# Optimization experiments

Measured on AMD Instinct MI355X. Metric: run time of the kernel, lower is better.

The kernel has to match this reference:

```python
import jax, jax.numpy as jnp
import numpy as np

EPS = 1e-5
COMMITMENT_WEIGHT = 1.0


def setup_inputs() -> dict:
    key = jax.random.key(0)
    k1, k2 = jax.random.split(key)
    x = jax.random.normal(k1, (4, 4096, 128), dtype=jnp.float32)
    codebook = jax.random.normal(k2, (8192, 128), dtype=jnp.float32)
    return {"x": x, "codebook": codebook}


def _layernorm(x):
    # LayerNorm over last dim, elementwise_affine=False, eps=1e-5
    mu = jnp.mean(x, axis=-1, keepdims=True)
    var = jnp.mean(jnp.square(x - mu), axis=-1, keepdims=True)
    return (x - mu) * jax.lax.rsqrt(var + EPS)


def reference(x, codebook):
    b, n, d = x.shape
    xn = _layernorm(x)                      # [b, n, d]
    flat = xn.reshape(b * n, d)             # [bn, d]
    x2 = jnp.sum(flat * flat, axis=-1, keepdims=True)          # [bn, 1]
    e2 = jnp.sum(codebook * codebook, axis=-1)                  # [K]
    dots = jnp.einsum('nd,kd->nk', flat, codebook)              # [bn, K]
    distances = x2 - 2.0 * dots + e2[None, :]                   # [bn, K]
    embed_ind = jnp.argmin(distances, axis=-1)                  # [bn]
    quantize = codebook[embed_ind].reshape(b, n, d)             # gather
    embed_ind = embed_ind.reshape(b, n)
    loss = jnp.mean(jnp.square(quantize - xn)) * COMMITMENT_WEIGHT
    # straight-through
    quantize_st = xn + jax.lax.stop_gradient(quantize - xn)
    return (quantize_st, embed_ind, loss)
```

## Files before the change

kernel.cpp:

```cpp
#include <hip/hip_runtime.h>
#include <hip/hip_fp16.h>
#include <math.h>

typedef _Float16 half8   __attribute__((ext_vector_type(8)));
typedef _Float16 half2v  __attribute__((ext_vector_type(2)));
typedef float    floatx16 __attribute__((ext_vector_type(16)));

#define ROWS   16384
#define DIM    128
#define KCODES 8192
#define NSPLIT 6
#define MTILE  128
#define LOSS_SCALE (1.0f / ((float)ROWS * (float)DIM))

__device__ __forceinline__ void async_copy16(const _Float16* src, _Float16* dst_lds) {
  __builtin_amdgcn_global_load_lds((const __attribute__((address_space(1))) void*)src,
                                   (__attribute__((address_space(3))) void*)dst_lds,
                                   16, 0, 0);
}

__global__ __launch_bounds__(256) void prep_codebook(
    const float* __restrict__ cb, _Float16* __restrict__ ehg,
    _Float16* __restrict__ elg, float* __restrict__ e2g)
{
  int tid = threadIdx.x;
  int L = tid & 63;
  int row = blockIdx.x * 4 + (tid >> 6);
  const float2* cr = (const float2*)(cb + (size_t)row * DIM);
  float2 v = cr[L];
  float s2 = v.x * v.x + v.y * v.y;
  #pragma unroll
  for (int m = 1; m < 64; m <<= 1) s2 += __shfl_xor(s2, m);
  if (L == 0) e2g[row] = -0.5f * s2;
  _Float16 h0 = (_Float16)v.x, h1 = (_Float16)v.y;
  half2v hi = {h0, h1};
  half2v lo = {(_Float16)(v.x - (float)h0), (_Float16)(v.y - (float)h1)};
  ((half2v*)(ehg + (size_t)row * DIM))[L] = hi;
  ((half2v*)(elg + (size_t)row * DIM))[L] = lo;
}

__global__ __launch_bounds__(256, 3) void argmin_kernel(
    const float* __restrict__ x, const _Float16* __restrict__ ehg,
    const _Float16* __restrict__ elg, const float* __restrict__ e2g,
    float* __restrict__ best_part, int* __restrict__ idx_part,
    float* __restrict__ x2g)
{
  __shared__ _Float16 ebuf[2][2][32][128];
  __shared__ float e2s[1376];

  int tid = threadIdx.x;
  int w   = tid >> 6;
  int L   = tid & 63;
  int col = L & 31;
  int kh  = L >> 5;

  int bx = blockIdx.x;
  int mt = bx & 127;
  int ns = bx >> 7;
  const int soff[7] = {0, 1376, 2752, 4128, 5504, 6848, 8192};
  int code0 = soff[ns];
  int ntile = (soff[ns + 1] - code0) >> 5;

  int rowbase = mt * MTILE + w * 32;
  int row = rowbase + col;

  for (int i = tid; i < soff[ns + 1] - code0; i += 256) e2s[i] = e2g[code0 + i];

  const float* xr = x + (size_t)row * DIM + kh * 8;
  float v[64];
  #pragma unroll
  for (int ks = 0; ks < 8; ++ks) {
    float4 p0 = *(const float4*)(xr + ks * 16);
    float4 p1 = *(const float4*)(xr + ks * 16 + 4);
    v[ks*8+0] = p0.x; v[ks*8+1] = p0.y; v[ks*8+2] = p0.z; v[ks*8+3] = p0.w;
    v[ks*8+4] = p1.x; v[ks*8+5] = p1.y; v[ks*8+6] = p1.z; v[ks*8+7] = p1.w;
  }
  float s = 0.f;
  #pragma unroll
  for (int i = 0; i < 64; ++i) s += v[i];
  s += __shfl_xor(s, 32);
  float mu = s * (1.0f / 128.0f);
  float s2 = 0.f;
  #pragma unroll
  for (int i = 0; i < 64; ++i) { float d = v[i] - mu; s2 += d * d; }
  s2 += __shfl_xor(s2, 32);
  float rstd = 1.0f / sqrtf(s2 * (1.0f / 128.0f) + 1e-5f);

  half8 ah[8], al[8];
  float x2 = 0.f;
  #pragma unroll
  for (int ks = 0; ks < 8; ++ks)
    #pragma unroll
    for (int j = 0; j < 8; ++j) {
      float xv = (v[ks*8+j] - mu) * rstd;
      x2 += xv * xv;
      _Float16 h = (_Float16)xv;
      ah[ks][j] = h;
      al[ks][j] = (_Float16)(xv - (float)h);
    }
  x2 += __shfl_xor(x2, 32);
  if (ns == 0 && kh == 0) x2g[row] = x2;

  float best[16]; int bch[16];
  #pragma unroll
  for (int r = 0; r < 16; ++r) { best[r] = -3.4e38f; bch[r] = 0; }

  auto stage = [&](int ch, int p) {
    int cbase = code0 + ch * 32;
    _Float16* lb = &ebuf[p][0][0][0];
    #pragma unroll
    for (int it = 0; it < 4; ++it) {
      int cid = it * 256 + tid;
      int arr = cid >> 9;
      int lc  = cid & 511;
      int n   = lc >> 4;
      int cs  = lc & 15;
      int cg  = cs ^ (n & 15);
      const _Float16* g = (arr ? elg : ehg) + (size_t)(cbase + n) * DIM + cg * 8;
      async_copy16(g, lb + (size_t)cid * 8);
    }
  };

  stage(0, 0);
  __syncthreads();

  for (int ch = 0; ch < ntile; ++ch) {
    int p = ch & 1;
    if (ch + 1 < ntile) stage(ch + 1, p ^ 1);

    float e2f = e2s[ch * 32 + col];

    floatx16 a0 = {0,0,0,0,0,0,0,0,0,0,0,0,0,0,0,0};
    floatx16 a1 = {0,0,0,0,0,0,0,0,0,0,0,0,0,0,0,0};
    #pragma unroll
    for (int ks = 0; ks < 8; ++ks) {
      int slot = (((ks << 1) | kh) ^ (col & 15)) * 8;
      half8 bh = *(const half8*)&ebuf[p][0][col][slot];
      half8 bl = *(const half8*)&ebuf[p][1][col][slot];
      a0 = __builtin_amdgcn_mfma_f32_32x32x16_f16(ah[ks], bh, a0, 0, 0, 0);
      a1 = __builtin_amdgcn_mfma_f32_32x32x16_f16(ah[ks], bl, a1, 0, 0, 0);
      a1 = __builtin_amdgcn_mfma_f32_32x32x16_f16(al[ks], bh, a1, 0, 0, 0);
    }
    #pragma unroll
    for (int r = 0; r < 16; ++r) {
      float t = (a0[r] + a1[r]) + e2f;
      if (t > best[r]) { best[r] = t; bch[r] = ch; }
    }
    __syncthreads();
  }

  int ibase = code0 + col;
  #pragma unroll
  for (int r = 0; r < 16; ++r) {
    float b = best[r];
    int   bi = (bch[r] << 5) + ibase;
    #pragma unroll
    for (int m = 1; m < 32; m <<= 1) {
      float ob = __shfl_xor(b, m);
      int   oi = __shfl_xor(bi, m);
      if (ob > b || (ob == b && oi < bi)) { b = ob; bi = oi; }
    }
    if (col == 0) {
      int rw = rowbase + (r & 3) + ((r >> 2) << 3) + (kh << 2);
      best_part[(size_t)rw * NSPLIT + ns] = b;
      idx_part [(size_t)rw * NSPLIT + ns] = bi;
    }
  }
}

__global__ __launch_bounds__(256) void gather_loss_kernel(
    const float* __restrict__ cb, const float* __restrict__ best_part,
    const int* __restrict__ idx_part, const float* __restrict__ x2g,
    float* __restrict__ out_q, float* __restrict__ out_ind,
    float* __restrict__ loss_part)
{
  __shared__ int   sidx[32];
  __shared__ float sloss[32];
  int tid = threadIdx.x;
  int rb = blockIdx.x * 32;
  int r = tid >> 3, k = tid & 7;
  int row = rb + r;

  float b  = -3.4e38f; int bi = 0x7fffffff;
  if (k < NSPLIT) {
    b  = best_part[(size_t)row * NSPLIT + k];
    bi = idx_part [(size_t)row * NSPLIT + k];
  }
  #pragma unroll
  for (int m = 1; m < 8; m <<= 1) {
    float ob = __shfl_xor(b, m);
    int   oi = __shfl_xor(bi, m);
    if (ob > b || (ob == b && oi < bi)) { b = ob; bi = oi; }
  }
  if (k == 0) {
    sidx[r] = bi;
    out_ind[row] = (float)bi;
    sloss[r] = x2g[row] - 2.0f * b;
  }
  __syncthreads();

  if (tid < 32) {
    float sl = sloss[tid];
    #pragma unroll
    for (int m = 1; m < 32; m <<= 1) sl += __shfl_xor(sl, m);
    if (tid == 0) loss_part[blockIdx.x] = sl;
  }

  const float4* cb4 = (const float4*)cb;
  float4* oq4 = (float4*)out_q;
  #pragma unroll
  for (int it = 0; it < 4; ++it) {
    int idx = it * 256 + tid;
    int r2 = idx >> 5, c4 = idx & 31;
    oq4[(size_t)(rb + r2) * 32 + c4] = cb4[(size_t)sidx[r2] * 32 + c4];
  }
}

__global__ __launch_bounds__(256) void loss_reduce_kernel(
    const float* __restrict__ loss_part, float* __restrict__ out_loss)
{
  __shared__ float sm[256];
  int tid = threadIdx.x;
  float s = loss_part[tid] + loss_part[tid + 256];
  sm[tid] = s; __syncthreads();
  for (int st = 128; st > 0; st >>= 1) {
    if (tid < st) sm[tid] += sm[tid + st];
    __syncthreads();
  }
  if (tid == 0) *out_loss = sm[0] * LOSS_SCALE;
}

extern "C" void kernel_launch(void* const* d_in, const int* in_sizes, int n_in,
                              void* d_out, int out_size, void* d_ws, size_t ws_size,
                              hipStream_t stream)
{
  const float* x  = (const float*)d_in[0];
  const float* cb = (const float*)d_in[1];

  char* ws = (char*)d_ws;
  _Float16* ehg      = (_Float16*)(ws + 0);
  _Float16* elg      = (_Float16*)(ws + 2097152);
  float*    e2g      = (float*)   (ws + 4194304);
  float*    best_part= (float*)   (ws + 4227072);
  int*      idx_part = (int*)     (ws + 4620288);
  float*    x2g      = (float*)   (ws + 5013504);
  float*    loss_part= (float*)   (ws + 5079040);

  float* out_q    = (float*)d_out;
  float* out_ind  = out_q + (size_t)ROWS * DIM;
  float* out_loss = out_ind + ROWS;

  prep_codebook<<<KCODES / 4, 256, 0, stream>>>(cb, ehg, elg, e2g);
  argmin_kernel<<<(ROWS / MTILE) * NSPLIT, 256, 0, stream>>>(x, ehg, elg, e2g, best_part, idx_part, x2g);
  gather_loss_kernel<<<ROWS / 32, 256, 0, stream>>>(cb, best_part, idx_part, x2g, out_q, out_ind, loss_part);
  loss_reduce_kernel<<<1, 256, 0, stream>>>(loss_part, out_loss);
}
```

Measured before the change: 179.3 us.

## Load codebook fragments directly from global memory, split layernorm into a prep kernel

Removes the LDS double-buffered async staging of codebook tiles. Each wave now reads its MFMA B fragments straight from global/L2 using an interleaved hi/lo fp16 layout. Layernorm and the fp16 hi/lo split of x move into a separate prep_x kernel, which writes into the output buffer as scratch. The K split drops from 6 to 4 with occupancy 2, and the gather kernel handles 64 rows per block. This removes LDS traffic and barriers, but every wave now fetches the codebook redundantly from L2, and it adds one launch.

```diff
diff --git a/kernel.cpp b/kernel.cpp
--- a/kernel.cpp
+++ b/kernel.cpp
@@ -9,25 +9,19 @@
 #define ROWS   16384
 #define DIM    128
 #define KCODES 8192
-#define NSPLIT 6
-#define MTILE  128
+#define NSPLIT 4
+#define SPLITK (KCODES / NSPLIT)
+#define NCH    (SPLITK / 32)
 #define LOSS_SCALE (1.0f / ((float)ROWS * (float)DIM))
 
-__device__ __forceinline__ void async_copy16(const _Float16* src, _Float16* dst_lds) {
-  __builtin_amdgcn_global_load_lds((const __attribute__((address_space(1))) void*)src,
-                                   (__attribute__((address_space(3))) void*)dst_lds,
-                                   16, 0, 0);
-}
-
-__global__ __launch_bounds__(256) void prep_codebook(
-    const float* __restrict__ cb, _Float16* __restrict__ ehg,
-    _Float16* __restrict__ elg, float* __restrict__ e2g)
+__global__ __launch_bounds__(256) void prep_cb(
+    const float* __restrict__ cb, _Float16* __restrict__ cbs,
+    float* __restrict__ e2g)
 {
   int tid = threadIdx.x;
   int L = tid & 63;
   int row = blockIdx.x * 4 + (tid >> 6);
-  const float2* cr = (const float2*)(cb + (size_t)row * DIM);
-  float2 v = cr[L];
+  float2 v = ((const float2*)(cb + (size_t)row * DIM))[L];
   float s2 = v.x * v.x + v.y * v.y;
   #pragma unroll
   for (int m = 1; m < 64; m <<= 1) s2 += __shfl_xor(s2, m);
@@ -35,18 +29,47 @@
   _Float16 h0 = (_Float16)v.x, h1 = (_Float16)v.y;
   half2v hi = {h0, h1};
   half2v lo = {(_Float16)(v.x - (float)h0), (_Float16)(v.y - (float)h1)};
-  ((half2v*)(ehg + (size_t)row * DIM))[L] = hi;
-  ((half2v*)(elg + (size_t)row * DIM))[L] = lo;
-}
-
-__global__ __launch_bounds__(256, 3) void argmin_kernel(
-    const float* __restrict__ x, const _Float16* __restrict__ ehg,
-    const _Float16* __restrict__ elg, const float* __restrict__ e2g,
-    float* __restrict__ best_part, int* __restrict__ idx_part,
+  _Float16* dst = cbs + (size_t)row * 256;
+  ((half2v*)dst)[L] = hi;
+  ((half2v*)(dst + 128))[L] = lo;
+}
+
+__global__ __launch_bounds__(256) void prep_x(
+    const float* __restrict__ x, _Float16* __restrict__ xs,
     float* __restrict__ x2g)
 {
-  __shared__ _Float16 ebuf[2][2][32][128];
-  __shared__ float e2s[1376];
+  int tid = threadIdx.x;
+  int L = tid & 63;
+  int row = blockIdx.x * 4 + (tid >> 6);
+  float2 v = ((const float2*)(x + (size_t)row * DIM))[L];
+  float s = v.x + v.y;
+  #pragma unroll
+  for (int m = 1; m < 64; m <<= 1) s += __shfl_xor(s, m);
+  float mu = s * (1.0f / 128.0f);
+  float dx = v.x - mu, dy = v.y - mu;
+  float s2 = dx * dx + dy * dy;
+  #pragma unroll
+  for (int m = 1; m < 64; m <<= 1) s2 += __shfl_xor(s2, m);
+  float rstd = 1.0f / sqrtf(s2 * (1.0f / 128.0f) + 1e-5f);
+  float xn0 = dx * rstd, xn1 = dy * rstd;
+  float x2 = xn0 * xn0 + xn1 * xn1;
+  #pragma unroll
+  for (int m = 1; m < 64; m <<= 1) x2 += __shfl_xor(x2, m);
+  if (L == 0) x2g[row] = x2;
+  _Float16 h0 = (_Float16)xn0, h1 = (_Float16)xn1;
+  half2v hi = {h0, h1};
+  half2v lo = {(_Float16)(xn0 - (float)h0), (_Float16)(xn1 - (float)h1)};
+  _Float16* dst = xs + (size_t)row * 256;
+  ((half2v*)dst)[L] = hi;
+  ((half2v*)(dst + 128))[L] = lo;
+}
+
+__global__ __launch_bounds__(256, 2) void argmin_kernel(
+    const _Float16* __restrict__ xs, const _Float16* __restrict__ cbs,
+    const float* __restrict__ e2g, float* __restrict__ best_part,
+    int* __restrict__ idx_part)
+{
+  __shared__ float e2s[SPLITK];
 
   int tid = threadIdx.x;
   int w   = tid >> 6;
@@ -54,99 +77,54 @@
   int col = L & 31;
   int kh  = L >> 5;
 
-  int bx = blockIdx.x;
-  int mt = bx & 127;
-  int ns = bx >> 7;
-  const int soff[7] = {0, 1376, 2752, 4128, 5504, 6848, 8192};
-  int code0 = soff[ns];
-  int ntile = (soff[ns + 1] - code0) >> 5;
-
-  int rowbase = mt * MTILE + w * 32;
-  int row = rowbase + col;
-
-  for (int i = tid; i < soff[ns + 1] - code0; i += 256) e2s[i] = e2g[code0 + i];
-
-  const float* xr = x + (size_t)row * DIM + kh * 8;
-  float v[64];
+  int mt = blockIdx.x & 127;
+  int ns = blockIdx.x >> 7;
+  int code0 = ns * SPLITK;
+
+  for (int i = tid; i < SPLITK; i += 256) e2s[i] = e2g[code0 + i];
+
+  int rowbase = mt * 128 + w * 32;
+
+  const _Float16* xa = xs + (size_t)(rowbase + col) * 256 + kh * 8;
+  half8 ah[8], al[8];
   #pragma unroll
   for (int ks = 0; ks < 8; ++ks) {
-    float4 p0 = *(const float4*)(xr + ks * 16);
-    float4 p1 = *(const float4*)(xr + ks * 16 + 4);
-    v[ks*8+0] = p0.x; v[ks*8+1] = p0.y; v[ks*8+2] = p0.z; v[ks*8+3] = p0.w;
-    v[ks*8+4] = p1.x; v[ks*8+5] = p1.y; v[ks*8+6] = p1.z; v[ks*8+7] = p1.w;
-  }
-  float s = 0.f;
-  #pragma unroll
-  for (int i = 0; i < 64; ++i) s += v[i];
-  s += __shfl_xor(s, 32);
-  float mu = s * (1.0f / 128.0f);
-  float s2 = 0.f;
-  #pragma unroll
-  for (int i = 0; i < 64; ++i) { float d = v[i] - mu; s2 += d * d; }
-  s2 += __shfl_xor(s2, 32);
-  float rstd = 1.0f / sqrtf(s2 * (1.0f / 128.0f) + 1e-5f);
-
-  half8 ah[8], al[8];
-  float x2 = 0.f;
-  #pragma unroll
-  for (int ks = 0; ks < 8; ++ks)
-    #pragma unroll
-    for (int j = 0; j < 8; ++j) {
-      float xv = (v[ks*8+j] - mu) * rstd;
-      x2 += xv * xv;
-      _Float16 h = (_Float16)xv;
-      ah[ks][j] = h;
-      al[ks][j] = (_Float16)(xv - (float)h);
-    }
-  x2 += __shfl_xor(x2, 32);
-  if (ns == 0 && kh == 0) x2g[row] = x2;
+    ah[ks] = *(const half8*)(xa + ks * 16);
+    al[ks] = *(const half8*)(xa + 128 + ks * 16);
+  }
 
   float best[16]; int bch[16];
   #pragma unroll
   for (int r = 0; r < 16; ++r) { best[r] = -3.4e38f; bch[r] = 0; }
 
-  auto stage = [&](int ch, int p) {
-    int cbase = code0 + ch * 32;
-    _Float16* lb = &ebuf[p][0][0][0];
-    #pragma unroll
-    for (int it = 0; it < 4; ++it) {
-      int cid = it * 256 + tid;
-      int arr = cid >> 9;
-      int lc  = cid & 511;
-      int n   = lc >> 4;
-      int cs  = lc & 15;
-      int cg  = cs ^ (n & 15);
-      const _Float16* g = (arr ? elg : ehg) + (size_t)(cbase + n) * DIM + cg * 8;
-      async_copy16(g, lb + (size_t)cid * 8);
-    }
-  };
-
-  stage(0, 0);
+  const _Float16* bp = cbs + (size_t)(code0 + col) * 256 + kh * 8;
+
   __syncthreads();
 
-  for (int ch = 0; ch < ntile; ++ch) {
-    int p = ch & 1;
-    if (ch + 1 < ntile) stage(ch + 1, p ^ 1);
-
+  #pragma unroll 1
+  for (int ch = 0; ch < NCH; ++ch) {
+    half8 bh[8], bl[8];
+    #pragma unroll
+    for (int ks = 0; ks < 8; ++ks) {
+      bh[ks] = *(const half8*)(bp + ks * 16);
+      bl[ks] = *(const half8*)(bp + 128 + ks * 16);
+    }
     float e2f = e2s[ch * 32 + col];
 
     floatx16 a0 = {0,0,0,0,0,0,0,0,0,0,0,0,0,0,0,0};
     floatx16 a1 = {0,0,0,0,0,0,0,0,0,0,0,0,0,0,0,0};
     #pragma unroll
     for (int ks = 0; ks < 8; ++ks) {
-      int slot = (((ks << 1) | kh) ^ (col & 15)) * 8;
-      half8 bh = *(const half8*)&ebuf[p][0][col][slot];
-      half8 bl = *(const half8*)&ebuf[p][1][col][slot];
-      a0 = __builtin_amdgcn_mfma_f32_32x32x16_f16(ah[ks], bh, a0, 0, 0, 0);
-      a1 = __builtin_amdgcn_mfma_f32_32x32x16_f16(ah[ks], bl, a1, 0, 0, 0);
-      a1 = __builtin_amdgcn_mfma_f32_32x32x16_f16(al[ks], bh, a1, 0, 0, 0);
+      a0 = __builtin_amdgcn_mfma_f32_32x32x16_f16(ah[ks], bh[ks], a0, 0, 0, 0);
+      a1 = __builtin_amdgcn_mfma_f32_32x32x16_f16(ah[ks], bl[ks], a1, 0, 0, 0);
+      a1 = __builtin_amdgcn_mfma_f32_32x32x16_f16(al[ks], bh[ks], a1, 0, 0, 0);
     }
     #pragma unroll
     for (int r = 0; r < 16; ++r) {
       float t = (a0[r] + a1[r]) + e2f;
       if (t > best[r]) { best[r] = t; bch[r] = ch; }
     }
-    __syncthreads();
+    bp += 32 * 256;
   }
 
   int ibase = code0 + col;
@@ -174,20 +152,17 @@
     float* __restrict__ out_q, float* __restrict__ out_ind,
     float* __restrict__ loss_part)
 {
-  __shared__ int   sidx[32];
-  __shared__ float sloss[32];
-  int tid = threadIdx.x;
-  int rb = blockIdx.x * 32;
-  int r = tid >> 3, k = tid & 7;
+  __shared__ int   sidx[64];
+  __shared__ float sloss[64];
+  int tid = threadIdx.x;
+  int rb = blockIdx.x * 64;
+  int r = tid >> 2, k = tid & 3;
   int row = rb + r;
 
-  float b  = -3.4e38f; int bi = 0x7fffffff;
-  if (k < NSPLIT) {
-    b  = best_part[(size_t)row * NSPLIT + k];
-    bi = idx_part [(size_t)row * NSPLIT + k];
-  }
-  #pragma unroll
-  for (int m = 1; m < 8; m <<= 1) {
+  float b  = best_part[(size_t)row * NSPLIT + k];
+  int   bi = idx_part [(size_t)row * NSPLIT + k];
+  #pragma unroll
+  for (int m = 1; m < 4; m <<= 1) {
     float ob = __shfl_xor(b, m);
     int   oi = __shfl_xor(bi, m);
     if (ob > b || (ob == b && oi < bi)) { b = ob; bi = oi; }
@@ -199,17 +174,17 @@
   }
   __syncthreads();
 
-  if (tid < 32) {
+  if (tid < 64) {
     float sl = sloss[tid];
     #pragma unroll
-    for (int m = 1; m < 32; m <<= 1) sl += __shfl_xor(sl, m);
+    for (int m = 1; m < 64; m <<= 1) sl += __shfl_xor(sl, m);
     if (tid == 0) loss_part[blockIdx.x] = sl;
   }
 
   const float4* cb4 = (const float4*)cb;
   float4* oq4 = (float4*)out_q;
   #pragma unroll
-  for (int it = 0; it < 4; ++it) {
+  for (int it = 0; it < 8; ++it) {
     int idx = it * 256 + tid;
     int r2 = idx >> 5, c4 = idx & 31;
     oq4[(size_t)(rb + r2) * 32 + c4] = cb4[(size_t)sidx[r2] * 32 + c4];
@@ -221,8 +196,8 @@
 {
   __shared__ float sm[256];
   int tid = threadIdx.x;
-  float s = loss_part[tid] + loss_part[tid + 256];
-  sm[tid] = s; __syncthreads();
+  sm[tid] = loss_part[tid];
+  __syncthreads();
   for (int st = 128; st > 0; st >>= 1) {
     if (tid < st) sm[tid] += sm[tid + st];
     __syncthreads();
@@ -238,20 +213,22 @@
   const float* cb = (const float*)d_in[1];
 
   char* ws = (char*)d_ws;
-  _Float16* ehg      = (_Float16*)(ws + 0);
-  _Float16* elg      = (_Float16*)(ws + 2097152);
+  _Float16* cbs      = (_Float16*)(ws + 0);
   float*    e2g      = (float*)   (ws + 4194304);
   float*    best_part= (float*)   (ws + 4227072);
-  int*      idx_part = (int*)     (ws + 4620288);
-  float*    x2g      = (float*)   (ws + 5013504);
-  float*    loss_part= (float*)   (ws + 5079040);
+  int*      idx_part = (int*)     (ws + 4489216);
+  float*    x2g      = (float*)   (ws + 4751360);
+  float*    loss_part= (float*)   (ws + 4816896);
 
   float* out_q    = (float*)d_out;
   float* out_ind  = out_q + (size_t)ROWS * DIM;
   float* out_loss = out_ind + ROWS;
 
-  prep_codebook<<<KCODES / 4, 256, 0, stream>>>(cb, ehg, elg, e2g);
-  argmin_kernel<<<(ROWS / MTILE) * NSPLIT, 256, 0, stream>>>(x, ehg, elg, e2g, best_part, idx_part, x2g);
-  gather_loss_kernel<<<ROWS / 32, 256, 0, stream>>>(cb, best_part, idx_part, x2g, out_q, out_ind, loss_part);
+  _Float16* xs = (_Float16*)out_q;
+
+  prep_cb<<<KCODES / 4, 256, 0, stream>>>(cb, cbs, e2g);
+  prep_x <<<ROWS / 4,  256, 0, stream>>>(x, xs, x2g);
+  argmin_kernel<<<128 * NSPLIT, 256, 0, stream>>>(xs, cbs, e2g, best_part, idx_part);
+  gather_loss_kernel<<<ROWS / 64, 256, 0, stream>>>(cb, best_part, idx_part, x2g, out_q, out_ind, loss_part);
   loss_reduce_kernel<<<1, 256, 0, stream>>>(loss_part, out_loss);
 }
```

Measured after the change: 312.2 us. 74.1% more time.
